# Kernel tuning notes

Measured on AMD Instinct MI355X. Metric: run time of the kernel, lower is better.

Reference implementation:

```python
import jax, jax.numpy as jnp
import numpy as np
import math

B, D, H = 16384, 1024, 8
NT, NC = 4, 16  # num tokens, num classes
DFF = 2 * D


def _ln(x, g, b, eps=1e-5):
    m = jnp.mean(x, axis=-1, keepdims=True)
    v = jnp.mean((x - m) ** 2, axis=-1, keepdims=True)
    return (x - m) / jnp.sqrt(v + eps) * g + b


def _mha(q_in, kv_in, wq, bq, wk, bk, wv, bv, wo, bo, mask=None):
    # q_in: (B, Sq, D), kv_in: (B, Sk, D)
    Bq, Sq, _ = q_in.shape
    dh = D // H
    q = (q_in @ wq.T + bq).reshape(Bq, Sq, H, dh).transpose(0, 2, 1, 3)
    k = (kv_in @ wk.T + bk).reshape(Bq, -1, H, dh).transpose(0, 2, 1, 3)
    v = (kv_in @ wv.T + bv).reshape(Bq, -1, H, dh).transpose(0, 2, 1, 3)
    s = jnp.einsum('bhqd,bhkd->bhqk', q, k) / math.sqrt(dh)
    if mask is not None:
        s = s + mask
    a = jax.nn.softmax(s, axis=-1)
    o = jnp.einsum('bhqk,bhkd->bhqd', a, v).transpose(0, 2, 1, 3).reshape(Bq, Sq, D)
    return o @ wo.T + bo


def setup_inputs() -> dict:
    key = jax.random.key(0)
    ks = jax.random.split(key, 24)
    nrm = lambda k, shp: jax.random.normal(k, shp, jnp.float32) * 0.02
    z = lambda *shp: jnp.zeros(shp, jnp.float32)
    o = lambda *shp: jnp.ones(shp, jnp.float32)
    return {
        'context': jax.random.normal(ks[0], (B, D), jnp.float32),
        'targets': jax.random.randint(ks[1], (B, NT), 0, NC),
        'tok_emb': nrm(ks[2], (NC + 1, D)),
        'pos_emb': nrm(ks[3], (NT, D)),
        'cp_ln_g': o(D), 'cp_ln_b': z(D),
        'cp_w': nrm(ks[4], (D, D)), 'cp_b': z(D),
        'sa_wq': nrm(ks[5], (D, D)), 'sa_bq': z(D),
        'sa_wk': nrm(ks[6], (D, D)), 'sa_bk': z(D),
        'sa_wv': nrm(ks[7], (D, D)), 'sa_bv': z(D),
        'sa_wo': nrm(ks[8], (D, D)), 'sa_bo': z(D),
        'ca_wq': nrm(ks[9], (D, D)), 'ca_bq': z(D),
        'ca_wk': nrm(ks[10], (D, D)), 'ca_bk': z(D),
        'ca_wv': nrm(ks[11], (D, D)), 'ca_bv': z(D),
        'ca_wo': nrm(ks[12], (D, D)), 'ca_bo': z(D),
        'ln1_g': o(D), 'ln1_b': z(D),
        'ln2_g': o(D), 'ln2_b': z(D),
        'ln3_g': o(D), 'ln3_b': z(D),
        'ff_w1': nrm(ks[13], (DFF, D)), 'ff_b1': z(DFF),
        'ff_w2': nrm(ks[14], (D, DFF)), 'ff_b2': z(D),
        'out_w': nrm(ks[15], (NC, D)), 'out_b': z(NC),
    }


def reference(context, targets, tok_emb, pos_emb, cp_ln_g, cp_ln_b, cp_w, cp_b,
              sa_wq, sa_bq, sa_wk, sa_bk, sa_wv, sa_bv, sa_wo, sa_bo,
              ca_wq, ca_bq, ca_wk, ca_bk, ca_wv, ca_bv, ca_wo, ca_bo,
              ln1_g, ln1_b, ln2_g, ln2_b, ln3_g, ln3_b,
              ff_w1, ff_b1, ff_w2, ff_b2, out_w, out_b):
    # context_proj: LN -> Linear -> GELU (exact); dropout is identity in eval
    mem = jax.nn.gelu(_ln(context, cp_ln_g, cp_ln_b) @ cp_w.T + cp_b, approximate=False)
    memory = mem[:, None, :]  # (B, 1, D)
    # teacher forcing: shift targets right, prepend start token (id = NC)
    start = jnp.full((context.shape[0], 1), NC, dtype=targets.dtype)
    shifted = jnp.concatenate([start, targets[:, :-1]], axis=1)  # (B, 4)
    x = tok_emb[shifted] + pos_emb[None]  # (B, 4, D)
    # causal mask (4, 4): -inf above diagonal
    mask = jnp.where(jnp.triu(jnp.ones((NT, NT), bool), 1), -jnp.inf, 0.0).astype(x.dtype)
    # TransformerDecoderLayer, norm_first=True, activation=relu (torch default)
    x = x + _mha(_ln(x, ln1_g, ln1_b), _ln(x, ln1_g, ln1_b),
                 sa_wq, sa_bq, sa_wk, sa_bk, sa_wv, sa_bv, sa_wo, sa_bo, mask=mask)
    x = x + _mha(_ln(x, ln2_g, ln2_b), memory,
                 ca_wq, ca_bq, ca_wk, ca_bk, ca_wv, ca_bv, ca_wo, ca_bo)
    h = _ln(x, ln3_g, ln3_b)
    x = x + (jax.nn.relu(h @ ff_w1.T + ff_b1) @ ff_w2.T + ff_b2)
    logits = x @ out_w.T + out_b  # (B, 4, 16)
    return logits
```

## Files before the change

### kernel.cpp

```cpp
#include <hip/hip_runtime.h>
#include <math.h>

typedef __bf16 bf16;
typedef float f32x4 __attribute__((ext_vector_type(4)));
typedef bf16 bf16x8 __attribute__((ext_vector_type(8)));
typedef bf16 bf16x4 __attribute__((ext_vector_type(4)));
typedef bf16 bf16x2 __attribute__((ext_vector_type(2)));

__device__ __forceinline__ void gll16(const void* g, void* l) {
    __builtin_amdgcn_global_load_lds(
        (const __attribute__((address_space(1))) void*)g,
        (__attribute__((address_space(3))) void*)l, 16, 0, 0);
}

struct CvtJobs {
    const float* s[9];
    bf16*        d[9];
    int          blk[10];
};

__global__ __launch_bounds__(256) void lam_cvt_all(CvtJobs J) {
    int b = blockIdx.x, j = 0;
    #pragma unroll
    for (int q = 1; q < 10; ++q) if (b >= J.blk[q]) j = q;
    const int i = (b - J.blk[j]) * 2048 + threadIdx.x * 8;
    const float* s = J.s[j];
    float4 a = *(const float4*)(s + i);
    float4 c = *(const float4*)(s + i + 4);
    bf16x8 o;
    o[0] = (bf16)a.x; o[1] = (bf16)a.y; o[2] = (bf16)a.z; o[3] = (bf16)a.w;
    o[4] = (bf16)c.x; o[5] = (bf16)c.y; o[6] = (bf16)c.z; o[7] = (bf16)c.w;
    *(bf16x8*)(J.d[j] + i) = o;
}

__global__ __launch_bounds__(256) void lam_packb(const float* __restrict__ q,
                                                 const float* __restrict__ k,
                                                 const float* __restrict__ v,
                                                 float* __restrict__ dst) {
    int i = blockIdx.x * 256 + threadIdx.x;
    if (i < 1024) dst[i] = q[i];
    else if (i < 2048) dst[i] = k[i - 1024];
    else if (i < 3072) dst[i] = v[i - 2048];
}

__global__ __launch_bounds__(256) void lam_transpose(const float* __restrict__ src,
                                                     bf16* __restrict__ dst) {
    __shared__ float tile[64][65];
    const int tid = threadIdx.x;
    const int bx = blockIdx.x * 64;
    const int by = blockIdx.y * 64;
    #pragma unroll
    for (int i = 0; i < 4; ++i) {
        const int r = (tid >> 4) + i * 16;
        const int c = (tid & 15) * 4;
        float4 v = *(const float4*)(src + (long)(by + r) * 1024 + bx + c);
        tile[r][c] = v.x; tile[r][c+1] = v.y; tile[r][c+2] = v.z; tile[r][c+3] = v.w;
    }
    __syncthreads();
    #pragma unroll
    for (int i = 0; i < 4; ++i) {
        const int r = (tid >> 4) + i * 16;
        const int c = (tid & 15) * 4;
        bf16x4 o;
        o[0] = (bf16)tile[c][r]; o[1] = (bf16)tile[c+1][r];
        o[2] = (bf16)tile[c+2][r]; o[3] = (bf16)tile[c+3][r];
        *(bf16x4*)(dst + (long)(bx + r) * 1024 + by + c) = o;
    }
}

__global__ __launch_bounds__(256) void lam_bcomb(const float* __restrict__ wo,
                                                 const float* __restrict__ bv,
                                                 const float* __restrict__ bo,
                                                 float* __restrict__ bcomb,
                                                 float* __restrict__ zb) {
    const int lane = threadIdx.x & 63;
    const int i = blockIdx.x * 4 + (threadIdx.x >> 6);
    float acc = 0.f;
    const float4* wp = (const float4*)(wo + (long)i * 1024);
    const float4* bp = (const float4*)bv;
    #pragma unroll
    for (int k = 0; k < 4; ++k) {
        const int q = lane + k * 64;
        float4 w = wp[q], b = bp[q];
        acc += w.x*b.x + w.y*b.y + w.z*b.z + w.w*b.w;
    }
    #pragma unroll
    for (int m = 32; m >= 1; m >>= 1) acc += __shfl_xor(acc, m);
    if (lane == 0) bcomb[i] = acc + bo[i];
    const int gid = blockIdx.x * 256 + threadIdx.x;
    if (gid < 1024) zb[gid] = 0.f;
}

__global__ __launch_bounds__(256) void lam_wof2(const bf16* __restrict__ Wout,
                                                const bf16* __restrict__ Wff2,
                                                bf16* __restrict__ Wof) {
    __shared__ bf16 wo[16 * 1024];
    __shared__ float red[16][16][16];
    const int tid = threadIdx.x;
    for (int i = tid * 8; i < 16384; i += 2048)
        *(bf16x8*)(wo + i) = *(const bf16x8*)(Wout + i);
    __syncthreads();
    const int cl = tid & 15;
    const int sl = tid >> 4;
    const long c = (long)blockIdx.x * 16 + cl;
    float acc[16] = {};
    for (int dd = 0; dd < 64; ++dd) {
        const int d = sl * 64 + dd;
        const float x = (float)Wff2[(long)d * 2048 + c];
        #pragma unroll
        for (int j = 0; j < 16; ++j) acc[j] += x * (float)wo[j * 1024 + d];
    }
    #pragma unroll
    for (int j = 0; j < 16; ++j) red[sl][cl][j] = acc[j];
    __syncthreads();
    const int rj = tid & 15, rc = tid >> 4;
    float s = 0.f;
    #pragma unroll
    for (int sl2 = 0; sl2 < 16; ++sl2) s += red[sl2][rc][rj];
    Wof[(long)rj * 2048 + blockIdx.x * 16 + rc] = (bf16)s;
}

__global__ __launch_bounds__(256) void lam_cb16(const bf16* __restrict__ Wout,
                                                const float* __restrict__ fb2,
                                                const float* __restrict__ ob,
                                                float* __restrict__ cb16) {
    const int lane = threadIdx.x & 63;
    const int j = blockIdx.x * 4 + (threadIdx.x >> 6);
    float acc = 0.f;
    #pragma unroll
    for (int m = 0; m < 16; ++m) {
        const int k = lane + m * 64;
        acc += (float)Wout[(long)j * 1024 + k] * fb2[k];
    }
    #pragma unroll
    for (int m = 32; m >= 1; m >>= 1) acc += __shfl_xor(acc, m);
    if (lane == 0) cb16[j] = acc + ob[j];
}

__global__ __launch_bounds__(256) void lam_dot16m(const bf16* __restrict__ X,
                                                  const bf16* __restrict__ Wo,
                                                  float* __restrict__ out, int M) {
    __shared__ bf16 ws[16 * 1024];
    const int tid = threadIdx.x;
    for (int i = tid * 8; i < 16384; i += 2048) {
        const int col = i >> 10, k = i & 1023;
        *(bf16x8*)(ws + col * 1024 + (k ^ ((col & 7) << 3))) = *(const bf16x8*)(Wo + i);
    }
    __syncthreads();

    const int lane = tid & 63;
    const int wid  = tid >> 6;
    const long rbase = (long)blockIdx.x * 64 + wid * 16;
    if (rbase >= M) return;
    const int cidx = lane & 15;
    const int kg   = lane >> 4;

    const bf16* ar = X + (rbase + cidx) * 1024 + kg * 8;
    const int bbase = cidx * 1024;
    const int bxor  = (cidx & 7) << 3;

    f32x4 acc = {};
    #pragma unroll 4
    for (int kt = 0; kt < 32; ++kt) {
        bf16x8 a = *(const bf16x8*)(ar + kt * 32);
        bf16x8 b = *(const bf16x8*)(ws + bbase + ((kt * 32 + kg * 8) ^ bxor));
        acc = __builtin_amdgcn_mfma_f32_16x16x32_bf16(a, b, acc, 0, 0, 0);
    }
    #pragma unroll
    for (int q = 0; q < 4; ++q) {
        const long r = rbase + kg * 4 + q;
        if (r < M) out[r * 16 + cidx] = acc[q];
    }
}

__global__ __launch_bounds__(256) void lam_dot16f(const float* __restrict__ Xv,
                                                  const bf16* __restrict__ Wo,
                                                  float* __restrict__ out, int M) {
    __shared__ bf16 ws[16 * 1032];
    const int tid = threadIdx.x;
    for (int i = tid * 8; i < 16384; i += 2048)
        *(bf16x8*)(ws + (i >> 10) * 1032 + (i & 1023)) = *(const bf16x8*)(Wo + i);
    __syncthreads();
    const int j = tid & 15;
    const bf16* wr = ws + j * 1032;
    #pragma unroll
    for (int rp = 0; rp < 4; ++rp) {
        const long r = (long)blockIdx.x * 64 + rp * 16 + (tid >> 4);
        if (r >= M) continue;
        float acc = 0.f;
        const float* xr = Xv + r * 1024;
        for (int k = 0; k < 1024; k += 4) {
            float4 xv = *(const float4*)(xr + k);
            acc += xv.x*(float)wr[k] + xv.y*(float)wr[k+1]
                 + xv.z*(float)wr[k+2] + xv.w*(float)wr[k+3];
        }
        out[r * 16 + j] = acc;
    }
}

__device__ __forceinline__ void ln_row(float (&v)[16], const float* g, const float* bta,
                                       int lane, bf16* out) {
    float s = 0.f;
    #pragma unroll
    for (int e = 0; e < 16; ++e) s += v[e];
    #pragma unroll
    for (int m = 32; m >= 1; m >>= 1) s += __shfl_xor(s, m);
    const float mean = s * (1.0f / 1024.0f);
    float vs = 0.f;
    #pragma unroll
    for (int e = 0; e < 16; ++e) { float d = v[e] - mean; vs += d * d; }
    #pragma unroll
    for (int m = 32; m >= 1; m >>= 1) vs += __shfl_xor(vs, m);
    const float rstd = rsqrtf(vs * (1.0f / 1024.0f) + 1e-5f);
    const int kb = lane * 16;
    const float4* gp = (const float4*)(g + kb);
    const float4* bp = (const float4*)(bta + kb);
    float r[16];
    #pragma unroll
    for (int q = 0; q < 4; ++q) {
        float4 a = gp[q], c = bp[q];
        r[q*4+0] = (v[q*4+0] - mean) * rstd * a.x + c.x;
        r[q*4+1] = (v[q*4+1] - mean) * rstd * a.y + c.y;
        r[q*4+2] = (v[q*4+2] - mean) * rstd * a.z + c.z;
        r[q*4+3] = (v[q*4+3] - mean) * rstd * a.w + c.w;
    }
    bf16x8 o0, o1;
    #pragma unroll
    for (int e = 0; e < 8; ++e) { o0[e] = (bf16)r[e]; o1[e] = (bf16)r[8+e]; }
    bf16x8* yp = (bf16x8*)out;
    yp[0] = o0; yp[1] = o1;
}

__global__ __launch_bounds__(256) void lam_ln_f32(const float* __restrict__ X,
                                                  const float* __restrict__ g,
                                                  const float* __restrict__ bta,
                                                  bf16* __restrict__ Y) {
    const int lane = threadIdx.x & 63;
    const long row = (long)blockIdx.x * 4 + (threadIdx.x >> 6);
    const long base = row * 1024 + lane * 16;
    float v[16];
    const float4* p = (const float4*)(X + base);
    #pragma unroll
    for (int q = 0; q < 4; ++q) {
        float4 f = p[q];
        v[q*4+0]=f.x; v[q*4+1]=f.y; v[q*4+2]=f.z; v[q*4+3]=f.w;
    }
    ln_row(v, g, bta, lane, Y + base);
}

__global__ __launch_bounds__(256) void lam_xtab(const float* __restrict__ tok,
                                                const float* __restrict__ pos,
                                                const float* __restrict__ g,
                                                const float* __restrict__ bta,
                                                float* __restrict__ xtab,
                                                bf16* __restrict__ ltab) {
    const int lane = threadIdx.x & 63;
    const int j = blockIdx.x * 4 + (threadIdx.x >> 6);
    if (j >= 68) return;
    const int t = j / 17, s = j % 17;
    float v[16];
    const float4* tp = (const float4*)(tok + (long)s * 1024 + lane * 16);
    const float4* pp = (const float4*)(pos + (long)t * 1024 + lane * 16);
    float4* xp = (float4*)(xtab + (long)j * 1024 + lane * 16);
    #pragma unroll
    for (int q = 0; q < 4; ++q) {
        float4 a = tp[q], c = pp[q];
        float4 o; o.x=a.x+c.x; o.y=a.y+c.y; o.z=a.z+c.z; o.w=a.w+c.w;
        xp[q] = o;
        v[q*4+0]=o.x; v[q*4+1]=o.y; v[q*4+2]=o.z; v[q*4+3]=o.w;
    }
    ln_row(v, g, bta, lane, ltab + (long)j * 1024 + lane * 16);
}

__global__ __launch_bounds__(256) void lam_attn_tab(const bf16* __restrict__ qkvtab,
                                                    bf16* __restrict__ atab) {
    const int lane = threadIdx.x & 63;
    const int unit = blockIdx.x * 4 + (threadIdx.x >> 6);
    const int u = unit >> 3, h = unit & 7;
    int t, s1 = 0, s2 = 0, s3 = 0;
    if (u == 0) { t = 0; }
    else if (u < 17) { t = 1; s1 = u - 1; }
    else if (u < 273) { t = 2; int v = u - 17; s1 = v >> 4; s2 = v & 15; }
    else { t = 3; int v = u - 273; s1 = v >> 8; s2 = (v >> 4) & 15; s3 = v & 15; }
    const int qs = (t == 0) ? 16 : (t == 1 ? s1 : (t == 2 ? s2 : s3));
    const int qrow = t * 17 + qs;
    const int krow[4] = { 16, 17 + s1, 34 + s2, 51 + s3 };
    const int base = h * 128 + lane * 2;

    bf16x2 qu = *(const bf16x2*)(qkvtab + (long)qrow * 3072 + base);
    const float q0 = (float)qu[0], q1 = (float)qu[1];
    float sc[4], v0[4], v1[4];
    #pragma unroll
    for (int j = 0; j < 4; ++j) {
        if (j <= t) {
            const bf16* kp = qkvtab + (long)krow[j] * 3072 + 1024 + base;
            bf16x2 ku = *(const bf16x2*)(kp);
            bf16x2 vu = *(const bf16x2*)(kp + 1024);
            sc[j] = q0 * (float)ku[0] + q1 * (float)ku[1];
            v0[j] = (float)vu[0]; v1[j] = (float)vu[1];
        } else { sc[j] = 0.f; v0[j] = 0.f; v1[j] = 0.f; }
    }
    #pragma unroll
    for (int m = 1; m < 64; m <<= 1)
        #pragma unroll
        for (int j = 0; j < 4; ++j)
            sc[j] += __shfl_xor(sc[j], m);
    const float scale = 0.08838834764831845f;
    float mx = -1e30f;
    #pragma unroll
    for (int j = 0; j < 4; ++j) if (j <= t) mx = fmaxf(mx, sc[j] * scale);
    float sum = 0.f, a[4];
    #pragma unroll
    for (int j = 0; j < 4; ++j) if (j <= t) { a[j] = expf(sc[j] * scale - mx); sum += a[j]; }
    const float inv = 1.0f / sum;
    float o0 = 0.f, o1 = 0.f;
    #pragma unroll
    for (int j = 0; j < 4; ++j) if (j <= t) { o0 += a[j] * inv * v0[j]; o1 += a[j] * inv * v1[j]; }
    bf16x2 ov; ov[0] = (bf16)o0; ov[1] = (bf16)o1;
    *(bf16x2*)(atab + (long)u * 1024 + base) = ov;
}

__global__ __launch_bounds__(256) void lam_gather_ln(const int* __restrict__ tg,
                                                     const float* __restrict__ xtab,
                                                     const bf16* __restrict__ aotab,
                                                     const bf16* __restrict__ caO,
                                                     const float* __restrict__ g,
                                                     const float* __restrict__ bta,
                                                     bf16* __restrict__ Y, long r0) {
    const int lane = threadIdx.x & 63;
    const long rl = (long)blockIdx.x * 4 + (threadIdx.x >> 6);
    const long r = r0 + rl;
    const long b = r >> 2;
    const int t = (int)(r & 3);
    const int tg0 = (t >= 1) ? tg[b*4] : 0;
    const int tg1 = (t >= 2) ? tg[b*4+1] : 0;
    const int tg2 = (t >= 3) ? tg[b*4+2] : 0;
    const int st = (t == 0) ? 16 : (t == 1 ? tg0 : (t == 2 ? tg1 : tg2));
    const long xrow = t * 17 + st;
    long idx;
    if (t == 0) idx = 0;
    else if (t == 1) idx = 1 + tg0;
    else if (t == 2) idx = 17 + tg0 * 16 + tg1;
    else idx = 273 + tg0 * 256 + tg1 * 16 + tg2;

    const int kb = lane * 16;
    float v[16];
    const float4* xp = (const float4*)(xtab + xrow * 1024 + kb);
    const bf16x8* ap = (const bf16x8*)(aotab + idx * 1024 + kb);
    const bf16x8* cp = (const bf16x8*)(caO + b * 1024 + kb);
    bf16x8 a0 = ap[0], a1 = ap[1], c0 = cp[0], c1 = cp[1];
    #pragma unroll
    for (int q = 0; q < 4; ++q) {
        float4 f = xp[q];
        v[q*4+0]=f.x; v[q*4+1]=f.y; v[q*4+2]=f.z; v[q*4+3]=f.w;
    }
    #pragma unroll
    for (int e = 0; e < 8; ++e) { v[e] += (float)a0[e] + (float)c0[e]; v[8+e] += (float)a1[e] + (float)c1[e]; }
    ln_row(v, g, bta, lane, Y + rl * 1024 + kb);
}

__global__ __launch_bounds__(256) void lam_logits16m(const bf16* __restrict__ q3,
                                                     const bf16* __restrict__ Wof,
                                                     const int* __restrict__ tg,
                                                     const float* __restrict__ xt16,
                                                     const float* __restrict__ ao16,
                                                     const float* __restrict__ ca16,
                                                     const float* __restrict__ cb16,
                                                     float* __restrict__ out, long r0) {
    __shared__ bf16 ws[16 * 2048];
    const int tid = threadIdx.x;
    for (int i = tid * 8; i < 32768; i += 2048) {
        const int col = i >> 11, k = i & 2047;
        *(bf16x8*)(ws + col * 2048 + (k ^ ((col & 7) << 3))) = *(const bf16x8*)(Wof + i);
    }
    __syncthreads();

    const int lane = tid & 63;
    const int wid  = tid >> 6;
    const long rbase = (long)blockIdx.x * 64 + wid * 16;
    const int cidx = lane & 15;
    const int kg   = lane >> 4;

    const bf16* ar = q3 + (rbase + cidx) * 2048 + kg * 8;
    const int bbase = cidx * 2048;
    const int bxor  = (cidx & 7) << 3;

    f32x4 acc = {};
    #pragma unroll 4
    for (int kt = 0; kt < 64; ++kt) {
        bf16x8 a = *(const bf16x8*)(ar + kt * 32);
        bf16x8 b = *(const bf16x8*)(ws + bbase + ((kt * 32 + kg * 8) ^ bxor));
        acc = __builtin_amdgcn_mfma_f32_16x16x32_bf16(a, b, acc, 0, 0, 0);
    }

    const float cbj = cb16[cidx];
    #pragma unroll
    for (int q = 0; q < 4; ++q) {
        const long rl = rbase + kg * 4 + q;
        const long r = r0 + rl;
        const long b = r >> 2;
        const int t = (int)(r & 3);
        const int tg0 = (t >= 1) ? tg[b*4] : 0;
        const int tg1 = (t >= 2) ? tg[b*4+1] : 0;
        const int tg2 = (t >= 3) ? tg[b*4+2] : 0;
        const int st = (t == 0) ? 16 : (t == 1 ? tg0 : (t == 2 ? tg1 : tg2));
        const long xrow = t * 17 + st;
        long idx;
        if (t == 0) idx = 0;
        else if (t == 1) idx = 1 + tg0;
        else if (t == 2) idx = 17 + tg0 * 16 + tg1;
        else idx = 273 + tg0 * 256 + tg1 * 16 + tg2;
        out[r * 16 + cidx] = acc[q] + xt16[xrow * 16 + cidx] + ao16[idx * 16 + cidx]
                           + ca16[b * 16 + cidx] + cbj;
    }
}

template<int EPI, int IM>
__device__ __forceinline__ void gemm_epi(f32x4 (&acc)[IM][4], const float* bias,
                                         bf16* C, const bf16* R,
                                         long bm, long bn, int wrow, int wcol,
                                         int lane, int N) {
    const int lr = (lane >> 4) * 4;
    const int lc = lane & 15;
    #pragma unroll
    for (int i = 0; i < IM; ++i) {
        const long row0 = bm + wrow + i * 16 + lr;
        #pragma unroll
        for (int j = 0; j < 4; ++j) {
            const long col = bn + wcol + j * 16 + lc;
            const float bvs = bias[col];
            #pragma unroll
            for (int qq = 0; qq < 4; ++qq) {
                const long row = row0 + qq;
                float v = acc[i][j][qq] + bvs;
                const long idx = row * N + col;
                if (EPI == 1) v = 0.5f * v * (1.0f + erff(v * 0.70710678118654752f));
                if (EPI == 2) v = fmaxf(v, 0.0f);
                if (EPI == 3) v += (float)R[idx];
                C[idx] = (bf16)v;
            }
        }
    }
}

template<int EPI, int TM>
__global__ __launch_bounds__(512, 2) void lam_gemm2(const bf16* __restrict__ A,
                                                    const bf16* __restrict__ W,
                                                    const float* __restrict__ bias,
                                                    bf16* C, const bf16* R,
                                                    int M, int N, int K) {
    constexpr int AR    = TM / 64;
    constexpr int ABYTE = TM * 128;
    constexpr int BUFB  = ABYTE + 32768;
    constexpr int IM    = TM / 32;
    __shared__ __attribute__((aligned(16))) char lds[2 * BUFB];

    const int t    = threadIdx.x;
    const int lane = t & 63;
    const int wid  = t >> 6;
    const int wm   = wid >> 2;
    const int wn   = wid & 3;

    const int gx   = gridDim.x;
    const int nwg  = gx * gridDim.y;
    const int orig = blockIdx.y * gx + blockIdx.x;
    const int q8 = nwg >> 3, r8 = nwg & 7;
    const int xcd = orig & 7, i8 = orig >> 3;
    const int wg  = (xcd < r8 ? xcd * (q8 + 1) : r8 * (q8 + 1) + (xcd - r8) * q8) + i8;
    const long bm = (long)(wg / gx) * TM;
    const long bn = (long)(wg % gx) * 256;

    const long rs = (long)K * 2;
    const char* Ag = (const char*)A + bm * rs;
    const char* Wg = (const char*)W + bn * rs;
    const int  srow = t >> 3;
    const int  scol = (((t & 7) ^ ((t >> 3) & 7)) << 4);
    const long g0   = (long)srow * rs + scol;

    const int xorq = (lane & 7) << 4;
    const int arow = wm * (TM / 2) + (lane & 15);
    const int brow = wn * 64 + (lane & 15);
    const int kq   = (lane >> 4) * 16;

    f32x4 acc[IM][4] = {};

    auto STAGE = [&](int buf, long kbyte) {
        char* base = lds + buf * BUFB + wid * 1024;
        const char* ga = Ag + g0 + kbyte;
        const char* gb = Wg + g0 + kbyte;
        #pragma unroll
        for (int r = 0; r < AR; ++r)
            gll16(ga + (long)r * 64 * rs, base + r * 8192);
        #pragma unroll
        for (int r = 0; r < 4; ++r)
            gll16(gb + (long)r * 64 * rs, base + ABYTE + r * 8192);
    };

    STAGE(0, 0);
    asm volatile("s_waitcnt vmcnt(0)" ::: "memory");
    __syncthreads();

    const int NT = K >> 6;
    int cur = 0;
    for (int kt = 0; kt < NT; ++kt) {
        if (kt + 1 < NT) STAGE(cur ^ 1, (long)(kt + 1) * 128);
        const char* ab = lds + cur * BUFB;
        const char* bb = ab + ABYTE;
        #pragma unroll
        for (int ks = 0; ks < 2; ++ks) {
            const int kc = kq + ks * 64;
            bf16x8 bvv[4];
            #pragma unroll
            for (int j = 0; j < 4; ++j) {
                const int x = (brow + j * 16) * 128 + kc;
                bvv[j] = *(const bf16x8*)(bb + (x ^ xorq));
            }
            #pragma unroll
            for (int i = 0; i < IM; ++i) {
                const int x = (arow + i * 16) * 128 + kc;
                bf16x8 avv = *(const bf16x8*)(ab + (x ^ xorq));
                #pragma unroll
                for (int j = 0; j < 4; ++j)
                    acc[i][j] = __builtin_amdgcn_mfma_f32_16x16x32_bf16(avv, bvv[j], acc[i][j], 0, 0, 0);
            }
        }
        asm volatile("s_waitcnt vmcnt(0)" ::: "memory");
        __syncthreads();
        cur ^= 1;
    }

    gemm_epi<EPI, IM>(acc, bias, C, R, bm, bn, wm * (TM / 2), wn * 64, lane, N);
}

static void gemm2(int epi, const bf16* A, const bf16* W, const float* bias, bf16* C,
                  const bf16* R, int M, int N, int K, hipStream_t s) {
    const long n256 = (long)(M >> 8) * (N >> 8);
    if (n256 >= 256 && (M & 255) == 0) {
        dim3 grid(N / 256, M / 256);
        switch (epi) {
            case 0: lam_gemm2<0,256><<<grid,512,0,s>>>(A,W,bias,C,R,M,N,K); break;
            case 1: lam_gemm2<1,256><<<grid,512,0,s>>>(A,W,bias,C,R,M,N,K); break;
            case 2: lam_gemm2<2,256><<<grid,512,0,s>>>(A,W,bias,C,R,M,N,K); break;
            default:lam_gemm2<3,256><<<grid,512,0,s>>>(A,W,bias,C,R,M,N,K); break;
        }
    } else {
        dim3 grid(N / 256, M / 128);
        switch (epi) {
            case 0: lam_gemm2<0,128><<<grid,512,0,s>>>(A,W,bias,C,R,M,N,K); break;
            case 1: lam_gemm2<1,128><<<grid,512,0,s>>>(A,W,bias,C,R,M,N,K); break;
            case 2: lam_gemm2<2,128><<<grid,512,0,s>>>(A,W,bias,C,R,M,N,K); break;
            default:lam_gemm2<3,128><<<grid,512,0,s>>>(A,W,bias,C,R,M,N,K); break;
        }
    }
}

extern "C" void kernel_launch(void* const* d_in, const int* in_sizes, int n_in,
                              void* d_out, int out_size, void* d_ws, size_t ws_size,
                              hipStream_t stream) {
    const float* context = (const float*)d_in[0];
    const int*   targets = (const int*)d_in[1];
    const float* tok_emb = (const float*)d_in[2];
    const float* pos_emb = (const float*)d_in[3];
    const float* cp_ln_g = (const float*)d_in[4];
    const float* cp_ln_b = (const float*)d_in[5];
    const float* cp_w    = (const float*)d_in[6];
    const float* cp_b    = (const float*)d_in[7];
    const float* sa_wq   = (const float*)d_in[8];
    const float* sa_bq   = (const float*)d_in[9];
    const float* sa_wk   = (const float*)d_in[10];
    const float* sa_bk   = (const float*)d_in[11];
    const float* sa_wv   = (const float*)d_in[12];
    const float* sa_bv   = (const float*)d_in[13];
    const float* sa_wo   = (const float*)d_in[14];
    const float* sa_bo   = (const float*)d_in[15];
    const float* ca_wv   = (const float*)d_in[20];
    const float* ca_bv   = (const float*)d_in[21];
    const float* ca_wo   = (const float*)d_in[22];
    const float* ca_bo   = (const float*)d_in[23];
    const float* ln1_g   = (const float*)d_in[24];
    const float* ln1_b   = (const float*)d_in[25];
    const float* ln3_g   = (const float*)d_in[28];
    const float* ln3_b   = (const float*)d_in[29];
    const float* ff_w1   = (const float*)d_in[30];
    const float* ff_b1   = (const float*)d_in[31];
    const float* ff_w2   = (const float*)d_in[32];
    const float* ff_b2   = (const float*)d_in[33];
    const float* out_w   = (const float*)d_in[34];
    const float* out_b   = (const float*)d_in[35];

    char* ws = (char*)d_ws;
    size_t off = 0;
    auto take = [&](size_t bytes) -> char* {
        char* p = ws + off;
        off += (bytes + 255) & ~(size_t)255;
        return p;
    };
    bf16*  Wcp   = (bf16*)take((size_t)1048576 * 2);
    bf16*  Wqkv  = (bf16*)take((size_t)3145728 * 2);
    bf16*  Wsao  = (bf16*)take((size_t)1048576 * 2);
    bf16*  Wcao  = (bf16*)take((size_t)1048576 * 2);
    bf16*  WvT   = (bf16*)take((size_t)1048576 * 2);
    bf16*  Wcomb = (bf16*)take((size_t)1048576 * 2);
    bf16*  Wff1  = (bf16*)take((size_t)2097152 * 2);
    bf16*  Wff2  = (bf16*)take((size_t)2097152 * 2);
    bf16*  Wout  = (bf16*)take((size_t)16384 * 2);
    bf16*  Wof   = (bf16*)take((size_t)32768 * 2);
    float* bqkv  = (float*)take((size_t)3072 * 4);
    float* bcomb = (float*)take((size_t)1024 * 4);
    float* zb    = (float*)take((size_t)1024 * 4);
    float* cb16  = (float*)take((size_t)16 * 4);
    float* xtab  = (float*)take((size_t)128 * 1024 * 4);
    bf16*  ltab  = (bf16*)take((size_t)128 * 1024 * 2);
    bf16*  qkvtab= (bf16*)take((size_t)128 * 3072 * 2);
    bf16*  atab  = (bf16*)take((size_t)4608 * 1024 * 2);
    bf16*  aotab = (bf16*)take((size_t)4608 * 1024 * 2);
    bf16*  caO   = (bf16*)take((size_t)16384 * 1024 * 2);
    float* xt16  = (float*)take((size_t)128 * 16 * 4);
    float* ao16  = (float*)take((size_t)4608 * 16 * 4);
    float* ca16  = (float*)take((size_t)16384 * 16 * 4);

    long chunk_rows = 65536;
    while (chunk_rows > 512 &&
           off + (size_t)chunk_rows * 6144 > ws_size)
        chunk_rows >>= 1;
    bf16* hb = (bf16*)take((size_t)chunk_rows * 1024 * 2);
    bf16* q3 = (bf16*)take((size_t)chunk_rows * 2048 * 2);
    const long nchunks = 65536 / chunk_rows;

    {
        CvtJobs J;
        const float* srcs[9] = { cp_w, sa_wq, sa_wk, sa_wv, sa_wo, ca_wo, ff_w1, ff_w2, out_w };
        bf16* dsts[9] = { Wcp, Wqkv, Wqkv + 1048576, Wqkv + 2097152, Wsao, Wcao, Wff1, Wff2, Wout };
        const int ns[9] = { 1048576, 1048576, 1048576, 1048576, 1048576, 1048576,
                            2097152, 2097152, 16384 };
        int cum = 0;
        for (int j = 0; j < 9; ++j) {
            J.s[j] = srcs[j]; J.d[j] = dsts[j];
            J.blk[j] = cum; cum += ns[j] / 2048;
        }
        J.blk[9] = cum;
        lam_cvt_all<<<cum, 256, 0, stream>>>(J);
    }
    lam_packb<<<12, 256, 0, stream>>>(sa_bq, sa_bk, sa_bv, bqkv);

    lam_transpose<<<dim3(16, 16), 256, 0, stream>>>(ca_wv, WvT);
    lam_bcomb<<<256, 256, 0, stream>>>(ca_wo, ca_bv, ca_bo, bcomb, zb);
    gemm2(0, Wcao, WvT, zb, Wcomb, nullptr, 1024, 1024, 1024, stream);
    lam_wof2<<<128, 256, 0, stream>>>(Wout, Wff2, Wof);
    lam_cb16<<<4, 256, 0, stream>>>(Wout, ff_b2, out_b, cb16);

    lam_xtab<<<17, 256, 0, stream>>>(tok_emb, pos_emb, ln1_g, ln1_b, xtab, ltab);
    gemm2(0, ltab, Wqkv, bqkv, qkvtab, nullptr, 128, 3072, 1024, stream);
    lam_attn_tab<<<8738, 256, 0, stream>>>(qkvtab, atab);
    gemm2(0, atab, Wsao, sa_bo, aotab, nullptr, 4608, 1024, 1024, stream);
    lam_dot16m<<<72, 256, 0, stream>>>(aotab, Wout, ao16, 4608);
    lam_dot16f<<<2, 256, 0, stream>>>(xtab, Wout, xt16, 68);

    const long cm = (chunk_rows < 16384) ? chunk_rows : 16384;
    for (long r0 = 0; r0 < 16384; r0 += cm) {
        lam_ln_f32<<<cm / 4, 256, 0, stream>>>(context + r0 * 1024, cp_ln_g, cp_ln_b, hb);
        gemm2(1, hb, Wcp, cp_b, q3, nullptr, (int)cm, 1024, 1024, stream);
        gemm2(0, q3, Wcomb, bcomb, caO + r0 * 1024, nullptr, (int)cm, 1024, 1024, stream);
    }
    lam_dot16m<<<256, 256, 0, stream>>>(caO, Wout, ca16, 16384);

    for (long c = 0; c < nchunks; ++c) {
        const long r0 = c * chunk_rows;
        lam_gather_ln<<<chunk_rows / 4, 256, 0, stream>>>(targets, xtab, aotab, caO,
                                                          ln3_g, ln3_b, hb, r0);
        gemm2(2, hb, Wff1, ff_b1, q3, nullptr, (int)chunk_rows, 2048, 1024, stream);
        lam_logits16m<<<chunk_rows / 64, 256, 0, stream>>>(q3, Wof, targets, xt16, ao16,
                                                           ca16, cb16, (float*)d_out, r0);
    }

    (void)in_sizes; (void)n_in; (void)out_size;
}
```

Measured before the change: 700.1 us.

## Fuse FF1 GEMM with ReLU and logits projection using atomic accumulation

Replaces the FF1 GEMM plus separate logits kernel with one kernel. It computes each 256x256 tile of relu(h@W1+b1), stages it in LDS as bf16, multiplies it by the folded Wof slice, and atomically adds the 16-wide partial logits into the output, which is zeroed beforehand. This removes the write and re-read of the large (rows x 2048) FF intermediate and drops the unused bf16 ff_w2 conversion, reading fp32 ff_w2 directly in the fold kernel. It also restructures the context chunk loop to use a dedicated buffer plus a device copy, and adds atomic contention across 8 column tiles along with a memset.

```diff
diff --git a/kernel.cpp b/kernel.cpp
--- a/kernel.cpp
+++ b/kernel.cpp
@@ -14,15 +14,15 @@
 }
 
 struct CvtJobs {
-    const float* s[9];
-    bf16*        d[9];
+    const float* s[8];
+    bf16*        d[8];
     int          blk[10];
 };
 
 __global__ __launch_bounds__(256) void lam_cvt_all(CvtJobs J) {
     int b = blockIdx.x, j = 0;
     #pragma unroll
-    for (int q = 1; q < 10; ++q) if (b >= J.blk[q]) j = q;
+    for (int q = 1; q < 8; ++q) if (b >= J.blk[q]) j = q;
     const int i = (b - J.blk[j]) * 2048 + threadIdx.x * 8;
     const float* s = J.s[j];
     float4 a = *(const float4*)(s + i);
@@ -92,7 +92,7 @@
 }
 
 __global__ __launch_bounds__(256) void lam_wof2(const bf16* __restrict__ Wout,
-                                                const bf16* __restrict__ Wff2,
+                                                const float* __restrict__ ff_w2,
                                                 bf16* __restrict__ Wof) {
     __shared__ bf16 wo[16 * 1024];
     __shared__ float red[16][16][16];
@@ -106,7 +106,7 @@
     float acc[16] = {};
     for (int dd = 0; dd < 64; ++dd) {
         const int d = sl * 64 + dd;
-        const float x = (float)Wff2[(long)d * 2048 + c];
+        const float x = ff_w2[(long)d * 2048 + c];
         #pragma unroll
         for (int j = 0; j < 16; ++j) acc[j] += x * (float)wo[j * 1024 + d];
     }
@@ -359,62 +359,6 @@
     ln_row(v, g, bta, lane, Y + rl * 1024 + kb);
 }
 
-__global__ __launch_bounds__(256) void lam_logits16m(const bf16* __restrict__ q3,
-                                                     const bf16* __restrict__ Wof,
-                                                     const int* __restrict__ tg,
-                                                     const float* __restrict__ xt16,
-                                                     const float* __restrict__ ao16,
-                                                     const float* __restrict__ ca16,
-                                                     const float* __restrict__ cb16,
-                                                     float* __restrict__ out, long r0) {
-    __shared__ bf16 ws[16 * 2048];
-    const int tid = threadIdx.x;
-    for (int i = tid * 8; i < 32768; i += 2048) {
-        const int col = i >> 11, k = i & 2047;
-        *(bf16x8*)(ws + col * 2048 + (k ^ ((col & 7) << 3))) = *(const bf16x8*)(Wof + i);
-    }
-    __syncthreads();
-
-    const int lane = tid & 63;
-    const int wid  = tid >> 6;
-    const long rbase = (long)blockIdx.x * 64 + wid * 16;
-    const int cidx = lane & 15;
-    const int kg   = lane >> 4;
-
-    const bf16* ar = q3 + (rbase + cidx) * 2048 + kg * 8;
-    const int bbase = cidx * 2048;
-    const int bxor  = (cidx & 7) << 3;
-
-    f32x4 acc = {};
-    #pragma unroll 4
-    for (int kt = 0; kt < 64; ++kt) {
-        bf16x8 a = *(const bf16x8*)(ar + kt * 32);
-        bf16x8 b = *(const bf16x8*)(ws + bbase + ((kt * 32 + kg * 8) ^ bxor));
-        acc = __builtin_amdgcn_mfma_f32_16x16x32_bf16(a, b, acc, 0, 0, 0);
-    }
-
-    const float cbj = cb16[cidx];
-    #pragma unroll
-    for (int q = 0; q < 4; ++q) {
-        const long rl = rbase + kg * 4 + q;
-        const long r = r0 + rl;
-        const long b = r >> 2;
-        const int t = (int)(r & 3);
-        const int tg0 = (t >= 1) ? tg[b*4] : 0;
-        const int tg1 = (t >= 2) ? tg[b*4+1] : 0;
-        const int tg2 = (t >= 3) ? tg[b*4+2] : 0;
-        const int st = (t == 0) ? 16 : (t == 1 ? tg0 : (t == 2 ? tg1 : tg2));
-        const long xrow = t * 17 + st;
-        long idx;
-        if (t == 0) idx = 0;
-        else if (t == 1) idx = 1 + tg0;
-        else if (t == 2) idx = 17 + tg0 * 16 + tg1;
-        else idx = 273 + tg0 * 256 + tg1 * 16 + tg2;
-        out[r * 16 + cidx] = acc[q] + xt16[xrow * 16 + cidx] + ao16[idx * 16 + cidx]
-                           + ca16[b * 16 + cidx] + cbj;
-    }
-}
-
 template<int EPI, int IM>
 __device__ __forceinline__ void gemm_epi(f32x4 (&acc)[IM][4], const float* bias,
                                          bf16* C, const bf16* R,
@@ -550,6 +494,159 @@
             case 1: lam_gemm2<1,128><<<grid,512,0,s>>>(A,W,bias,C,R,M,N,K); break;
             case 2: lam_gemm2<2,128><<<grid,512,0,s>>>(A,W,bias,C,R,M,N,K); break;
             default:lam_gemm2<3,128><<<grid,512,0,s>>>(A,W,bias,C,R,M,N,K); break;
+        }
+    }
+}
+
+__global__ __launch_bounds__(512, 2) void lam_gemm_fl(const bf16* __restrict__ A,
+                                                      const bf16* __restrict__ W,
+                                                      const float* __restrict__ bias,
+                                                      const bf16* __restrict__ Wof,
+                                                      const int* __restrict__ tg,
+                                                      const float* __restrict__ xt16,
+                                                      const float* __restrict__ ao16,
+                                                      const float* __restrict__ ca16,
+                                                      const float* __restrict__ cb16,
+                                                      float* __restrict__ out,
+                                                      long r0, int K) {
+    constexpr int ABYTE = 32768;
+    constexpr int BUFB  = 65536;
+    __shared__ __attribute__((aligned(16))) char lds[2 * BUFB];
+
+    const int t    = threadIdx.x;
+    const int lane = t & 63;
+    const int wid  = t >> 6;
+    const int wm   = wid >> 2;
+    const int wn   = wid & 3;
+
+    const int gx   = gridDim.x;
+    const int nwg  = gx * gridDim.y;
+    const int orig = blockIdx.y * gx + blockIdx.x;
+    const int q8 = nwg >> 3, r8 = nwg & 7;
+    const int xcd = orig & 7, i8 = orig >> 3;
+    const int wg  = (xcd < r8 ? xcd * (q8 + 1) : r8 * (q8 + 1) + (xcd - r8) * q8) + i8;
+    const long bm = (long)(wg / gx) * 256;
+    const long bn = (long)(wg % gx) * 256;
+
+    const long rs = (long)K * 2;
+    const char* Ag = (const char*)A + bm * rs;
+    const char* Wg = (const char*)W + bn * rs;
+    const int  srow = t >> 3;
+    const int  scol = (((t & 7) ^ ((t >> 3) & 7)) << 4);
+    const long g0   = (long)srow * rs + scol;
+
+    const int xorq = (lane & 7) << 4;
+    const int arow = wm * 128 + (lane & 15);
+    const int brow = wn * 64 + (lane & 15);
+    const int kq   = (lane >> 4) * 16;
+
+    f32x4 acc[8][4] = {};
+
+    auto STAGE = [&](int buf, long kbyte) {
+        char* base = lds + buf * BUFB + wid * 1024;
+        const char* ga = Ag + g0 + kbyte;
+        const char* gb = Wg + g0 + kbyte;
+        #pragma unroll
+        for (int r = 0; r < 4; ++r)
+            gll16(ga + (long)r * 64 * rs, base + r * 8192);
+        #pragma unroll
+        for (int r = 0; r < 4; ++r)
+            gll16(gb + (long)r * 64 * rs, base + ABYTE + r * 8192);
+    };
+
+    STAGE(0, 0);
+    asm volatile("s_waitcnt vmcnt(0)" ::: "memory");
+    __syncthreads();
+
+    const int NT = K >> 6;
+    int cur = 0;
+    for (int kt = 0; kt < NT; ++kt) {
+        if (kt + 1 < NT) STAGE(cur ^ 1, (long)(kt + 1) * 128);
+        const char* ab = lds + cur * BUFB;
+        const char* bb = ab + ABYTE;
+        #pragma unroll
+        for (int ks = 0; ks < 2; ++ks) {
+            const int kc = kq + ks * 64;
+            bf16x8 bvv[4];
+            #pragma unroll
+            for (int j = 0; j < 4; ++j) {
+                const int x = (brow + j * 16) * 128 + kc;
+                bvv[j] = *(const bf16x8*)(bb + (x ^ xorq));
+            }
+            #pragma unroll
+            for (int i = 0; i < 8; ++i) {
+                const int x = (arow + i * 16) * 128 + kc;
+                bf16x8 avv = *(const bf16x8*)(ab + (x ^ xorq));
+                #pragma unroll
+                for (int j = 0; j < 4; ++j)
+                    acc[i][j] = __builtin_amdgcn_mfma_f32_16x16x32_bf16(avv, bvv[j], acc[i][j], 0, 0, 0);
+            }
+        }
+        asm volatile("s_waitcnt vmcnt(0)" ::: "memory");
+        __syncthreads();
+        cur ^= 1;
+    }
+
+    {
+        const int lr = (lane >> 4) * 4;
+        const int lc = lane & 15;
+        #pragma unroll
+        for (int i = 0; i < 8; ++i) {
+            const int row0 = wm * 128 + i * 16 + lr;
+            #pragma unroll
+            for (int j = 0; j < 4; ++j) {
+                const int col = wn * 64 + j * 16 + lc;
+                const float bvs = bias[bn + col];
+                #pragma unroll
+                for (int qq = 0; qq < 4; ++qq) {
+                    const int row = row0 + qq;
+                    const float v = fmaxf(acc[i][j][qq] + bvs, 0.0f);
+                    *(bf16*)(lds + row * 512 + ((col * 2) ^ ((row & 7) << 4))) = (bf16)v;
+                }
+            }
+        }
+    }
+    __syncthreads();
+
+    const int cidx = lane & 15;
+    const int kg   = lane >> 4;
+    f32x4 acc2[2] = {};
+    #pragma unroll
+    for (int kt = 0; kt < 8; ++kt) {
+        bf16x8 bfrag = *(const bf16x8*)(Wof + (long)cidx * 2048 + bn + kt * 32 + kg * 8);
+        #pragma unroll
+        for (int rt = 0; rt < 2; ++rt) {
+            const int row = wid * 32 + rt * 16 + cidx;
+            const int kby = (kt * 32 + kg * 8) * 2;
+            bf16x8 afrag = *(const bf16x8*)(lds + row * 512 + (kby ^ ((row & 7) << 4)));
+            acc2[rt] = __builtin_amdgcn_mfma_f32_16x16x32_bf16(afrag, bfrag, acc2[rt], 0, 0, 0);
+        }
+    }
+
+    #pragma unroll
+    for (int rt = 0; rt < 2; ++rt) {
+        #pragma unroll
+        for (int q = 0; q < 4; ++q) {
+            const long rl = bm + wid * 32 + rt * 16 + kg * 4 + q;
+            const long r = r0 + rl;
+            float v = acc2[rt][q];
+            if (bn == 0) {
+                const long b = r >> 2;
+                const int tt = (int)(r & 3);
+                const int tg0 = (tt >= 1) ? tg[b*4] : 0;
+                const int tg1 = (tt >= 2) ? tg[b*4+1] : 0;
+                const int tg2 = (tt >= 3) ? tg[b*4+2] : 0;
+                const int st = (tt == 0) ? 16 : (tt == 1 ? tg0 : (tt == 2 ? tg1 : tg2));
+                const long xrow = tt * 17 + st;
+                long idx;
+                if (tt == 0) idx = 0;
+                else if (tt == 1) idx = 1 + tg0;
+                else if (tt == 2) idx = 17 + tg0 * 16 + tg1;
+                else idx = 273 + tg0 * 256 + tg1 * 16 + tg2;
+                v += xt16[xrow * 16 + cidx] + ao16[idx * 16 + cidx]
+                   + ca16[b * 16 + cidx] + cb16[cidx];
+            }
+            atomicAdd(&out[r * 16 + cidx], v);
         }
     }
 }
@@ -602,7 +699,6 @@
     bf16*  WvT   = (bf16*)take((size_t)1048576 * 2);
     bf16*  Wcomb = (bf16*)take((size_t)1048576 * 2);
     bf16*  Wff1  = (bf16*)take((size_t)2097152 * 2);
-    bf16*  Wff2  = (bf16*)take((size_t)2097152 * 2);
     bf16*  Wout  = (bf16*)take((size_t)16384 * 2);
     bf16*  Wof   = (bf16*)take((size_t)32768 * 2);
     float* bqkv  = (float*)take((size_t)3072 * 4);
@@ -618,27 +714,27 @@
     float* xt16  = (float*)take((size_t)128 * 16 * 4);
     float* ao16  = (float*)take((size_t)4608 * 16 * 4);
     float* ca16  = (float*)take((size_t)16384 * 16 * 4);
+    bf16*  cbuf  = (bf16*)take((size_t)16384 * 1024 * 2);
 
     long chunk_rows = 65536;
     while (chunk_rows > 512 &&
-           off + (size_t)chunk_rows * 6144 > ws_size)
+           off + (size_t)chunk_rows * 2048 > ws_size)
         chunk_rows >>= 1;
     bf16* hb = (bf16*)take((size_t)chunk_rows * 1024 * 2);
-    bf16* q3 = (bf16*)take((size_t)chunk_rows * 2048 * 2);
     const long nchunks = 65536 / chunk_rows;
 
     {
         CvtJobs J;
-        const float* srcs[9] = { cp_w, sa_wq, sa_wk, sa_wv, sa_wo, ca_wo, ff_w1, ff_w2, out_w };
-        bf16* dsts[9] = { Wcp, Wqkv, Wqkv + 1048576, Wqkv + 2097152, Wsao, Wcao, Wff1, Wff2, Wout };
-        const int ns[9] = { 1048576, 1048576, 1048576, 1048576, 1048576, 1048576,
-                            2097152, 2097152, 16384 };
+        const float* srcs[8] = { cp_w, sa_wq, sa_wk, sa_wv, sa_wo, ca_wo, ff_w1, out_w };
+        bf16* dsts[8] = { Wcp, Wqkv, Wqkv + 1048576, Wqkv + 2097152, Wsao, Wcao, Wff1, Wout };
+        const int ns[8] = { 1048576, 1048576, 1048576, 1048576, 1048576, 1048576,
+                            2097152, 16384 };
         int cum = 0;
-        for (int j = 0; j < 9; ++j) {
+        for (int j = 0; j < 8; ++j) {
             J.s[j] = srcs[j]; J.d[j] = dsts[j];
             J.blk[j] = cum; cum += ns[j] / 2048;
         }
-        J.blk[9] = cum;
+        J.blk[8] = cum; J.blk[9] = cum;
         lam_cvt_all<<<cum, 256, 0, stream>>>(J);
     }
     lam_packb<<<12, 256, 0, stream>>>(sa_bq, sa_bk, sa_bv, bqkv);
@@ -646,7 +742,7 @@
     lam_transpose<<<dim3(16, 16), 256, 0, stream>>>(ca_wv, WvT);
     lam_bcomb<<<256, 256, 0, stream>>>(ca_wo, ca_bv, ca_bo, bcomb, zb);
     gemm2(0, Wcao, WvT, zb, Wcomb, nullptr, 1024, 1024, 1024, stream);
-    lam_wof2<<<128, 256, 0, stream>>>(Wout, Wff2, Wof);
+    lam_wof2<<<128, 256, 0, stream>>>(Wout, ff_w2, Wof);
     lam_cb16<<<4, 256, 0, stream>>>(Wout, ff_b2, out_b, cb16);
 
     lam_xtab<<<17, 256, 0, stream>>>(tok_emb, pos_emb, ln1_g, ln1_b, xtab, ltab);
@@ -656,21 +752,23 @@
     lam_dot16m<<<72, 256, 0, stream>>>(aotab, Wout, ao16, 4608);
     lam_dot16f<<<2, 256, 0, stream>>>(xtab, Wout, xt16, 68);
 
-    const long cm = (chunk_rows < 16384) ? chunk_rows : 16384;
-    for (long r0 = 0; r0 < 16384; r0 += cm) {
-        lam_ln_f32<<<cm / 4, 256, 0, stream>>>(context + r0 * 1024, cp_ln_g, cp_ln_b, hb);
-        gemm2(1, hb, Wcp, cp_b, q3, nullptr, (int)cm, 1024, 1024, stream);
-        gemm2(0, q3, Wcomb, bcomb, caO + r0 * 1024, nullptr, (int)cm, 1024, 1024, stream);
+    for (long r0 = 0; r0 < 16384; r0 += 16384) {
+        lam_ln_f32<<<4096, 256, 0, stream>>>(context + r0 * 1024, cp_ln_g, cp_ln_b, cbuf);
+        gemm2(1, cbuf, Wcp, cp_b, (bf16*)caO + r0 * 1024, nullptr, 16384, 1024, 1024, stream);
+        gemm2(0, (bf16*)caO + r0 * 1024, Wcomb, bcomb, cbuf, nullptr, 16384, 1024, 1024, stream);
+        hipMemcpyAsync(caO + r0 * 1024, cbuf, (size_t)16384 * 1024 * 2,
+                       hipMemcpyDeviceToDevice, stream);
     }
     lam_dot16m<<<256, 256, 0, stream>>>(caO, Wout, ca16, 16384);
 
+    hipMemsetAsync(d_out, 0, (size_t)65536 * 16 * 4, stream);
     for (long c = 0; c < nchunks; ++c) {
         const long r0 = c * chunk_rows;
         lam_gather_ln<<<chunk_rows / 4, 256, 0, stream>>>(targets, xtab, aotab, caO,
                                                           ln3_g, ln3_b, hb, r0);
-        gemm2(2, hb, Wff1, ff_b1, q3, nullptr, (int)chunk_rows, 2048, 1024, stream);
-        lam_logits16m<<<chunk_rows / 64, 256, 0, stream>>>(q3, Wof, targets, xt16, ao16,
-                                                           ca16, cb16, (float*)d_out, r0);
+        lam_gemm_fl<<<dim3(8, chunk_rows / 256), 512, 0, stream>>>(
+            hb, Wff1, ff_b1, Wof, targets, xt16, ao16, ca16, cb16,
+            (float*)d_out, r0, 1024);
     }
 
     (void)in_sizes; (void)n_in; (void)out_size;
```

Measured after the change: 646.8 us. 1.08x faster.
